# Optimization experiments

Measured on AMD Instinct MI355X. Metric: run time of the kernel, lower is better.

The kernel has to match this reference:

```python
import jax, jax.numpy as jnp
import numpy as np

T_TOK, N_UNITS, E, H, L_PATH, N_PATHS, B, VOCAB = 16, 4096, 128, 128, 32, 1024, 8, 16384
MAX_PATH_LEN = 32
PAD_ID = 0


def _run_lstm(x, Wi, Wh, b):
    # x: [T, N, E]; torch gate order i, f, g, o
    Hh = Wh.shape[1]
    h0 = jnp.zeros((x.shape[1], Hh), x.dtype)
    def step(carry, xt):
        h, c = carry
        g = xt @ Wi.T + h @ Wh.T + b
        i, f, gg, o = jnp.split(g, 4, axis=-1)
        c = jax.nn.sigmoid(f) * c + jax.nn.sigmoid(i) * jnp.tanh(gg)
        h = jax.nn.sigmoid(o) * jnp.tanh(c)
        return (h, c), h
    _, ys = jax.lax.scan(step, (h0, h0), x)
    return ys


def _bilstm(x, lengths, Wif, Whf, bf, Wib, Whb, bb):
    # emulates pack_padded_sequence + bidirectional LSTM + pad_packed (zeros past length)
    T = x.shape[0]
    t = jnp.arange(T)[:, None]
    valid = t < lengths[None, :]
    out_f = _run_lstm(x, Wif, Whf, bf)
    rev = jnp.clip(lengths[None, :] - 1 - t, 0, T - 1)  # reverse within each valid prefix
    x_rev = jnp.take_along_axis(x, rev[:, :, None], axis=0)
    out_b = jnp.take_along_axis(_run_lstm(x_rev, Wib, Whb, bb), rev[:, :, None], axis=0)
    return jnp.concatenate([out_f, out_b], axis=-1) * valid[:, :, None]


def _layernorm(x, g, b):
    m = x.mean(-1, keepdims=True)
    v = ((x - m) ** 2).mean(-1, keepdims=True)
    return (x - m) * jax.lax.rsqrt(v + 1e-5) * g + b


def _forward(units, paths, unit_per_data, path_per_data, emb, tl_Wif, tl_Whf, tl_bf,
             tl_Wib, tl_Whb, tl_bb, lin_W, lin_b, ln_g, ln_b, attn_w, attn_b,
             pl_Wif, pl_Whf, pl_bf, pl_Wib, pl_Whb, pl_bb, ul_W, ul_b):
    # ---- _token_encoder ----
    is_pad = units == PAD_ID
    tok_len = jnp.where(is_pad.any(0), jnp.argmax(is_pad, 0), units.shape[0])
    x = emb[units]                                              # [T, NU, E]
    h = _bilstm(x, tok_len, tl_Wif, tl_Whf, tl_bf, tl_Wib, tl_Whb, tl_bb)  # [T, NU, 2H]
    out = h @ lin_W.T + lin_b                                   # [T, NU, E]
    q = jnp.tanh(_layernorm(out, ln_g, ln_b))
    scores = q @ attn_w.T + attn_b                              # [T, NU, 1] local attention
    scores = jnp.where(is_pad[:, :, None], -1e9, scores)
    w = jax.nn.softmax(scores, axis=0)
    tok_feat = jnp.einsum('tn,tne->ne', w[..., 0], out)         # [NU, E]
    # ---- _unit_to_path (vectorized ragged gather) ----
    Lp, Pn = paths.shape
    has_end = (paths == -1).any(0)
    fe = jnp.where(has_end, jnp.argmax(paths == -1, 0), Lp)
    ML = min(Lp, MAX_PATH_LEN)
    nb = unit_per_data.shape[0]
    data_of_path = jnp.repeat(jnp.arange(nb), path_per_data, total_repeat_length=Pn)
    u_off = jnp.cumsum(unit_per_data) - unit_per_data
    off_p = u_off[data_of_path]
    un_p = unit_per_data[data_of_path]
    pL = paths[:ML]
    t = jnp.arange(ML)[:, None]
    within = t < fe[None, :]
    keep = within & (pL >= 0) & (pL < un_p[None, :])
    gidx = jnp.clip(jnp.clip(pL, 0, None) + off_p[None, :], 0, tok_feat.shape[0] - 1)
    feats = tok_feat[gidx] * keep[:, :, None]                   # [ML, P, E]
    mask = jnp.where(within, (pL < 0) | (pL > un_p[None, :]), True)
    # ---- _path_encoder ----
    p_len = jnp.where(mask.any(0), jnp.argmax(mask, 0), ML)
    hp = _bilstm(feats, p_len, pl_Wif, pl_Whf, pl_bf, pl_Wib, pl_Whb, pl_bb)
    return hp @ ul_W.T + ul_b                                   # [ML, P, E]


def setup_inputs() -> dict:
    rng = np.random.default_rng(0)
    tok_len = rng.integers(4, T_TOK + 1, N_UNITS); tok_len[0] = T_TOK
    units = rng.integers(1, VOCAB, (T_TOK, N_UNITS))
    units = np.where(np.arange(T_TOK)[:, None] < tok_len[None, :], units, PAD_ID)
    upd = N_UNITS // B
    p_len = rng.integers(8, L_PATH + 1, N_PATHS); p_len[0] = L_PATH
    paths = rng.integers(0, upd, (L_PATH, N_PATHS))
    paths = np.where(np.arange(L_PATH)[:, None] < p_len[None, :], paths, -1)
    key = jax.random.key(0)
    ks = iter(jax.random.split(key, 24))
    def pn(shape, s=0.08):
        return (jax.random.normal(next(ks), shape) * s).astype(jnp.float32)
    return dict(
        units=jnp.asarray(units, jnp.int32),
        paths=jnp.asarray(paths, jnp.int32),
        unit_per_data=jnp.full((B,), upd, jnp.int32),
        path_per_data=jnp.full((B,), N_PATHS // B, jnp.int32),
        emb=pn((VOCAB, E)),
        tl_Wif=pn((4 * H, E)), tl_Whf=pn((4 * H, H)), tl_bf=pn((4 * H,)),
        tl_Wib=pn((4 * H, E)), tl_Whb=pn((4 * H, H)), tl_bb=pn((4 * H,)),
        lin_W=pn((E, 2 * H)), lin_b=pn((E,)),
        ln_g=jnp.ones((E,), jnp.float32), ln_b=jnp.zeros((E,), jnp.float32),
        attn_w=pn((1, E)), attn_b=pn((1,)),
        pl_Wif=pn((4 * H, E)), pl_Whf=pn((4 * H, H)), pl_bf=pn((4 * H,)),
        pl_Wib=pn((4 * H, E)), pl_Whb=pn((4 * H, H)), pl_bb=pn((4 * H,)),
        ul_W=pn((E, 2 * H)), ul_b=pn((E,)),
    )


def reference(units, paths, unit_per_data, path_per_data, emb, tl_Wif, tl_Whf, tl_bf,
              tl_Wib, tl_Whb, tl_bb, lin_W, lin_b, ln_g, ln_b, attn_w, attn_b,
              pl_Wif, pl_Whf, pl_bf, pl_Wib, pl_Whb, pl_bb, ul_W, ul_b):
    return _forward(units, paths, unit_per_data, path_per_data, emb, tl_Wif, tl_Whf, tl_bf,
                    tl_Wib, tl_Whb, tl_bb, lin_W, lin_b, ln_g, ln_b, attn_w, attn_b,
                    pl_Wif, pl_Whf, pl_bf, pl_Wib, pl_Whb, pl_bb, ul_W, ul_b)
```

## Files before the change

kernel.cpp:

```cpp
#include <hip/hip_runtime.h>
#include <cstdint>
#include <cstddef>

#define T_TOKN 16
#define NUNITS 4096
#define LPATH  32
#define NPATHS 1024
#define BNUM   8

typedef __attribute__((ext_vector_type(8))) short short8;
typedef __attribute__((ext_vector_type(4))) short short4x;
typedef __attribute__((ext_vector_type(4))) float f32x4;

enum : size_t {
  OFF_WFRAG   = 0,
  OFF_LINFRAG = 262144,
  OFF_OUTF    = 294912,
  OFF_OUTB    = OFF_OUTF + 4194304,
  OFF_OUTLIN  = OFF_OUTB + 4194304,
  OFF_SCORES  = OFF_OUTLIN + 8388608,
  OFF_TOKFEAT = OFF_SCORES + 65536,
  OFF_POUTF   = OFF_TOKFEAT + 524288,
  OFF_POUTB   = OFF_POUTF + 2097152,
  OFF_INT     = OFF_POUTB + 2097152,
  WS_FLOATS   = OFF_INT + 8192
};

static __device__ __forceinline__ unsigned short f2bf(float f) {
  union { float f; unsigned u; } v; v.f = f;
  unsigned r = v.u + 0x7fffu + ((v.u >> 16) & 1u);
  return (unsigned short)(r >> 16);
}
static __device__ __forceinline__ unsigned pack_bf(float a, float b) {
  return (unsigned)f2bf(a) | ((unsigned)f2bf(b) << 16);
}
static __device__ __forceinline__ float sigf(float x)      { return 1.f / (1.f + __expf(-x)); }
static __device__ __forceinline__ float tanhfast(float x)  { return 2.f / (1.f + __expf(-2.f * x)) - 1.f; }

__global__ void prep_kernel(
    const float* __restrict__ tWif, const float* __restrict__ tWhf,
    const float* __restrict__ tWib, const float* __restrict__ tWhb,
    const float* __restrict__ pWif, const float* __restrict__ pWhf,
    const float* __restrict__ pWib, const float* __restrict__ pWhb,
    const float* __restrict__ linW, const float* __restrict__ ulW,
    const int* __restrict__ units, const int* __restrict__ paths,
    const int* __restrict__ upd, const int* __restrict__ ppd,
    float* __restrict__ ws, int* __restrict__ ip)
{
  int idx = blockIdx.x * 256 + threadIdx.x;
  if (idx < 524288) {
    unsigned short* wf = (unsigned short*)(ws + OFF_WFRAG);
    int mat = idx >> 17, rem = idx & 131071;
    int i  = rem & 7;
    int lane = (rem >> 3) & 63;
    int ct = (rem >> 9) & 3;
    int ks = (rem >> 11) & 7;
    int wv = (rem >> 14) & 7;
    int g = wv * 64 + ct * 16 + (lane & 15);
    int k = ks * 32 + ((lane >> 4) << 3) + i;
    const float* Wi; const float* Wh;
    switch (mat) {
      case 0: Wi = tWif; Wh = tWhf; break;
      case 1: Wi = tWib; Wh = tWhb; break;
      case 2: Wi = pWif; Wh = pWhf; break;
      default: Wi = pWib; Wh = pWhb; break;
    }
    float v = (k < 128) ? Wi[g * 128 + k] : Wh[g * 128 + (k - 128)];
    wf[idx] = f2bf(v);
  } else if (idx < 524288 + 65536) {
    unsigned short* lf = (unsigned short*)(ws + OFF_LINFRAG);
    int i2 = idx - 524288;
    int mat = i2 >> 15, rem = i2 & 32767;
    int i  = rem & 7;
    int lane = (rem >> 3) & 63;
    int ks = (rem >> 9) & 7;
    int ct = (rem >> 12) & 7;
    int e = ct * 16 + (lane & 15);
    int k = ks * 32 + ((lane >> 4) << 3) + i;
    const float* W = mat ? ulW : linW;
    lf[i2] = f2bf(W[e * 256 + k]);
  } else if (idx < 589824 + 4096) {
    int n = idx - 589824;
    int len = T_TOKN;
    for (int t = 0; t < T_TOKN; ++t)
      if (units[t * NUNITS + n] == 0) { len = t; break; }
    ip[n] = len;
  } else if (idx < 589824 + 5120) {
    int p = idx - (589824 + 4096);
    int* fe_a  = ip + 4096;
    int* p_len = ip + 5120;
    int* off_p = ip + 6144;
    int* un_p  = ip + 7168;
    int cum = 0; int d = BNUM - 1;
    for (int dd = 0; dd < BNUM; ++dd) {
      int c2 = cum + ppd[dd];
      if (p < c2) { d = dd; break; }
      cum = c2;
    }
    int off = 0;
    for (int dd = 0; dd < d; ++dd) off += upd[dd];
    int un = upd[d];
    off_p[p] = off; un_p[p] = un;
    int f = LPATH;
    for (int t = 0; t < LPATH; ++t)
      if (paths[t * NPATHS + p] == -1) { f = t; break; }
    fe_a[p] = f;
    int pl = LPATH;
    for (int t = 0; t < LPATH; ++t) {
      int v = paths[t * NPATHS + p];
      if ((t >= f) || (v < 0) || (v > un)) { pl = t; break; }
    }
    p_len[p] = pl;
  }
}

template <int MODE>
__global__ __launch_bounds__(1024, 4) void lstm_kernel(
    const unsigned short* __restrict__ wfragAll,
    const float* __restrict__ biasF, const float* __restrict__ biasB,
    const float* __restrict__ src,
    const int* __restrict__ idxsrc,
    const int* __restrict__ lens,
    const int* __restrict__ fe_a, const int* __restrict__ off_p, const int* __restrict__ un_p,
    unsigned short* __restrict__ outF, unsigned short* __restrict__ outB)
{
  constexpr int NN   = MODE ? NPATHS : NUNITS;
  constexpr int TT   = MODE ? LPATH : T_TOKN;
  constexpr int M    = MODE ? 8 : 32;
  constexpr int MR   = MODE ? 16 : 32;
  constexpr int NRT  = MR / 16;
  constexpr int ASTR = 264;
  constexpr int GSTR = 514;

  __shared__ unsigned short ash[MR * ASTR];
  __shared__ float gates[MR * GSTR];

  int tid  = threadIdx.x;
  int dir  = blockIdx.y;
  int n0   = blockIdx.x * M;
  int lane = tid & 63, wv = tid >> 6;

  const unsigned short* wbase =
      wfragAll + (size_t)((MODE ? 2 : 0) + dir) * 131072;
  int wv8 = wv >> 1;
  short8 bfr[8][2];
#pragma unroll
  for (int ks = 0; ks < 8; ++ks)
#pragma unroll
    for (int c2 = 0; c2 < 2; ++c2) {
      int ct = ((wv & 1) << 1) | c2;
      bfr[ks][c2] = *(const short8*)&wbase[((((wv8 * 8 + ks) * 4 + ct) * 64) + lane) * 8];
    }

  if (MODE == 0) {
    for (int i = tid; i < MR * 128; i += 1024)
      ash[(i >> 7) * ASTR + 128 + (i & 127)] = 0;
  } else {
    for (int i = tid; i < MR * ASTR; i += 1024) ash[i] = 0;
  }

  const float* bcp = dir ? biasB : biasF;
  int j2 = MODE ? (tid & 127) : ((tid & 63) * 2);
  int ug = MODE ? (tid >> 7)  : (tid >> 6);
  float2 b2[4];
#pragma unroll
  for (int q = 0; q < 4; ++q) {
    if (MODE == 0) b2[q] = *(const float2*)&bcp[q * 128 + j2];
    else           b2[q] = make_float2(bcp[q * 128 + j2], 0.f);
  }
  constexpr int NU = MODE ? 1 : 2;
  float cst0[NU], cst1[NU];
  int   ulen[NU];
#pragma unroll
  for (int i = 0; i < NU; ++i) {
    cst0[i] = 0.f; cst1[i] = 0.f;
    ulen[i] = lens[n0 + ug * NU + i];
  }

  int gu, gk0;
  if (MODE == 0) { gu = tid >> 5; gk0 = (tid & 31) * 4; }
  else           { gu = tid >> 7; gk0 = tid & 127; }
  int gn = n0 + gu;
  int glen = lens[gn];
  int gfe = 0, goff = 0, gun = 0;
  if (MODE) { gfe = fe_a[gn]; goff = off_p[gn]; gun = un_p[gn]; }

  float4 xq; float xs;
  if (MODE == 0) {
    int tau = dir ? min(max(glen - 1, 0), TT - 1) : 0;
    int tok = idxsrc[tau * NN + gn];
    xq = *(const float4*)&src[(size_t)tok * 128 + gk0];
  } else {
    int tau = dir ? min(max(glen - 1, 0), TT - 1) : 0;
    int v = idxsrc[tau * NN + gn];
    bool keep = (tau < gfe) && (v >= 0) && (v < gun);
    xs = 0.f;
    if (keep) xs = src[(size_t)min(v + goff, NUNITS - 1) * 128 + gk0];
  }
  __syncthreads();

  for (int t = 0; t < TT; ++t) {
    if (MODE == 0) {
      short4x x4;
      x4[0] = (short)f2bf(xq.x); x4[1] = (short)f2bf(xq.y);
      x4[2] = (short)f2bf(xq.z); x4[3] = (short)f2bf(xq.w);
      *(short4x*)&ash[gu * ASTR + gk0] = x4;
    } else {
      ash[gu * ASTR + gk0] = f2bf(xs);
    }
    __syncthreads();

    {
      int tn = (t + 1 < TT) ? t + 1 : t;
      int taun = dir ? min(max(glen - 1 - tn, 0), TT - 1) : tn;
      int vn = idxsrc[taun * NN + gn];
      f32x4 acc[NRT][2];
#pragma unroll
      for (int rt = 0; rt < NRT; ++rt)
#pragma unroll
        for (int c2 = 0; c2 < 2; ++c2) {
          f32x4 z = {0.f, 0.f, 0.f, 0.f};
          acc[rt][c2] = z;
        }
#pragma unroll
      for (int ks = 0; ks < 8; ++ks) {
        short8 afr[NRT];
#pragma unroll
        for (int rt = 0; rt < NRT; ++rt)
          afr[rt] = *(const short8*)&ash[(rt * 16 + (lane & 15)) * ASTR + ks * 32 + ((lane >> 4) << 3)];
#pragma unroll
        for (int rt = 0; rt < NRT; ++rt)
#pragma unroll
          for (int c2 = 0; c2 < 2; ++c2)
            acc[rt][c2] = __builtin_amdgcn_mfma_f32_16x16x32_bf16(
                afr[rt], bfr[ks][c2], acc[rt][c2], 0, 0, 0);
      }
      if (MODE == 0) {
        xq = *(const float4*)&src[(size_t)vn * 128 + gk0];
      } else {
        bool keep = (taun < gfe) && (vn >= 0) && (vn < gun);
        xs = 0.f;
        if (keep) xs = src[(size_t)min(vn + goff, NUNITS - 1) * 128 + gk0];
      }
#pragma unroll
      for (int rt = 0; rt < NRT; ++rt)
#pragma unroll
        for (int c2 = 0; c2 < 2; ++c2) {
          int g = wv * 32 + c2 * 16 + (lane & 15);
#pragma unroll
          for (int r = 0; r < 4; ++r) {
            int u = rt * 16 + ((lane >> 4) << 2) + r;
            gates[u * GSTR + g] = acc[rt][c2][r];
          }
        }
    }
    __syncthreads();

#pragma unroll
    for (int i = 0; i < NU; ++i) {
      int u = ug * NU + i;
      int n = n0 + u;
      if (MODE == 0) {
        float2 g0 = *(const float2*)&gates[u * GSTR + j2];
        float2 g1 = *(const float2*)&gates[u * GSTR + 128 + j2];
        float2 g2 = *(const float2*)&gates[u * GSTR + 256 + j2];
        float2 g3 = *(const float2*)&gates[u * GSTR + 384 + j2];
        float i0 = sigf(g0.x + b2[0].x), i1 = sigf(g0.y + b2[0].y);
        float f0 = sigf(g1.x + b2[1].x), f1 = sigf(g1.y + b2[1].y);
        float c0 = tanhfast(g2.x + b2[2].x), c1 = tanhfast(g2.y + b2[2].y);
        float o0 = sigf(g3.x + b2[3].x), o1 = sigf(g3.y + b2[3].y);
        float cA = f0 * cst0[i] + i0 * c0;
        float cB = f1 * cst1[i] + i1 * c1;
        cst0[i] = cA; cst1[i] = cB;
        float h0 = o0 * tanhfast(cA);
        float h1 = o1 * tanhfast(cB);
        unsigned hp = pack_bf(h0, h1);
        *(unsigned*)&ash[u * ASTR + 128 + j2] = hp;
        if (dir == 0) {
          *(unsigned*)&outF[((size_t)t * NN + n) * 128 + j2] = hp;
        } else {
          int L = ulen[i];
          if (t < L) *(unsigned*)&outB[((size_t)(L - 1 - t) * NN + n) * 128 + j2] = hp;
          else       *(unsigned*)&outB[((size_t)t * NN + n) * 128 + j2] = 0;
        }
      } else {
        float p0 = gates[u * GSTR + j2]       + b2[0].x;
        float p1 = gates[u * GSTR + 128 + j2] + b2[1].x;
        float p2 = gates[u * GSTR + 256 + j2] + b2[2].x;
        float p3 = gates[u * GSTR + 384 + j2] + b2[3].x;
        float ig = sigf(p0), fg = sigf(p1), gg = tanhfast(p2), og = sigf(p3);
        float c = fg * cst0[i] + ig * gg;
        cst0[i] = c;
        float h = og * tanhfast(c);
        unsigned short hb = f2bf(h);
        ash[u * ASTR + 128 + j2] = hb;
        if (dir == 0) {
          outF[((size_t)t * NN + n) * 128 + j2] = hb;
        } else {
          int L = ulen[i];
          if (t < L) outB[((size_t)(L - 1 - t) * NN + n) * 128 + j2] = hb;
          else       outB[((size_t)t * NN + n) * 128 + j2] = 0;
        }
      }
    }
  }
}

template <int EPI>
__global__ __launch_bounds__(256) void gemm_mfma(
    const unsigned short* __restrict__ INf, const unsigned short* __restrict__ INb,
    const int* __restrict__ lens,
    const unsigned short* __restrict__ Bfrag, const float* __restrict__ bias,
    float* __restrict__ OUT, float* __restrict__ scores,
    const float* __restrict__ lng, const float* __restrict__ lnb,
    const float* __restrict__ attw, const float* __restrict__ attb,
    const int* __restrict__ units, int Nn)
{
  constexpr int OSTR = 132;
  __shared__ float outs[64 * OSTR];
  __shared__ float red1[256];
  __shared__ float red2[256];
  __shared__ float rowm[64], rowr[64];
  __shared__ float awsh[128], lgsh[128], lbsh[128];

  int tid = threadIdx.x, lane = tid & 63, wv = tid >> 6;
  int row0 = blockIdx.x * 64;
  int t = row0 / Nn, n0 = row0 % Nn;

  if (EPI == 1 && tid < 128) {
    awsh[tid] = attw[tid]; lgsh[tid] = lng[tid]; lbsh[tid] = lnb[tid];
  }

  short8 bfr[8][2];
#pragma unroll
  for (int ks = 0; ks < 8; ++ks)
#pragma unroll
    for (int c2 = 0; c2 < 2; ++c2) {
      int ct = wv * 2 + c2;
      bfr[ks][c2] = *(const short8*)&Bfrag[(((ct * 8 + ks) * 64) + lane) * 8];
    }

  int rb = lane & 15;
  int koq = (lane >> 4) << 3;
  bool val[4];
#pragma unroll
  for (int rt = 0; rt < 4; ++rt)
    val[rt] = (EPI == 1) ? true : (t < lens[n0 + rt * 16 + rb]);

  f32x4 acc[4][2];
#pragma unroll
  for (int rt = 0; rt < 4; ++rt)
#pragma unroll
    for (int c2 = 0; c2 < 2; ++c2) {
      f32x4 z = {0.f, 0.f, 0.f, 0.f};
      acc[rt][c2] = z;
    }

#pragma unroll
  for (int ks = 0; ks < 8; ++ks) {
    const unsigned short* P = (ks < 4) ? INf : INb;
    int koff = (ks & 3) * 32 + koq;
#pragma unroll
    for (int rt = 0; rt < 4; ++rt) {
      short8 a = {0, 0, 0, 0, 0, 0, 0, 0};
      if (val[rt])
        a = *(const short8*)&P[((size_t)(row0 + rt * 16 + rb)) * 128 + koff];
#pragma unroll
      for (int c2 = 0; c2 < 2; ++c2)
        acc[rt][c2] = __builtin_amdgcn_mfma_f32_16x16x32_bf16(
            a, bfr[ks][c2], acc[rt][c2], 0, 0, 0);
    }
  }

  float bc[2];
#pragma unroll
  for (int c2 = 0; c2 < 2; ++c2) bc[c2] = bias[wv * 32 + c2 * 16 + rb];
#pragma unroll
  for (int rt = 0; rt < 4; ++rt)
#pragma unroll
    for (int c2 = 0; c2 < 2; ++c2) {
      int col = wv * 32 + c2 * 16 + rb;
      int ub  = rt * 16 + ((lane >> 4) << 2);
#pragma unroll
      for (int r = 0; r < 4; ++r)
        outs[(ub + r) * OSTR + col] = acc[rt][c2][r] + bc[c2];
    }
  __syncthreads();
// ... 25 lines not shown
      rowm[tid] = m;
      rowr[tid] = rsqrtf(var + 1e-5f);
    }
    __syncthreads();
    float m = rowm[row], rs = rowr[row];
    float sp = 0.f;
#pragma unroll
    for (int x = 0; x < 8; ++x) {
#pragma unroll
      for (int c = 0; c < 4; ++c) {
        int col = seg * 32 + x * 4 + c;
        float q = tanhfast((v[x][c] - m) * rs * lgsh[col] + lbsh[col]);
        sp += q * awsh[col];
      }
      *(f32x4*)&OUT[go + x * 4] = v[x];
    }
    red1[tid] = sp;
    __syncthreads();
    if (tid < 64) {
      float s3 = red1[tid * 4] + red1[tid * 4 + 1] + red1[tid * 4 + 2] + red1[tid * 4 + 3]
               + attb[0];
      int n = n0 + tid;
      if (units[t * NUNITS + n] == 0) s3 = -1e9f;
      scores[t * NUNITS + n] = s3;
    }
  }
}

__global__ __launch_bounds__(128) void softmax_feat_kernel(
    const float* __restrict__ scores, const float* __restrict__ out_lin,
    float* __restrict__ tok_feat)
{
  int n = blockIdx.x;
  int e = threadIdx.x;
  float s[T_TOKN];
  float m = -1e30f;
#pragma unroll
  for (int t = 0; t < T_TOKN; ++t) { s[t] = scores[t * NUNITS + n]; m = fmaxf(m, s[t]); }
  float sum = 0.f;
#pragma unroll
  for (int t = 0; t < T_TOKN; ++t) { s[t] = expf(s[t] - m); sum += s[t]; }
  float inv = 1.f / sum;
  float a = 0.f;
#pragma unroll
  for (int t = 0; t < T_TOKN; ++t)
    a += s[t] * inv * out_lin[((size_t)t * NUNITS + n) * 128 + e];
  tok_feat[n * 128 + e] = a;
}

extern "C" void kernel_launch(void* const* d_in, const int* in_sizes, int n_in,
                              void* d_out, int out_size, void* d_ws, size_t ws_size,
                              hipStream_t stream)
{
  const int*   units = (const int*)d_in[0];
  const int*   paths = (const int*)d_in[1];
  const int*   upd   = (const int*)d_in[2];
  const int*   ppd   = (const int*)d_in[3];
  const float* emb   = (const float*)d_in[4];
  const float* tWif  = (const float*)d_in[5];
  const float* tWhf  = (const float*)d_in[6];
  const float* tbf   = (const float*)d_in[7];
  const float* tWib  = (const float*)d_in[8];
  const float* tWhb  = (const float*)d_in[9];
  const float* tbb   = (const float*)d_in[10];
  const float* linW  = (const float*)d_in[11];
  const float* linb  = (const float*)d_in[12];
  const float* lng   = (const float*)d_in[13];
  const float* lnb   = (const float*)d_in[14];
  const float* attw  = (const float*)d_in[15];
  const float* attb  = (const float*)d_in[16];
  const float* pWif  = (const float*)d_in[17];
  const float* pWhf  = (const float*)d_in[18];
  const float* pbf   = (const float*)d_in[19];
  const float* pWib  = (const float*)d_in[20];
  const float* pWhb  = (const float*)d_in[21];
  const float* pbb   = (const float*)d_in[22];
  const float* ulW   = (const float*)d_in[23];
  const float* ulb   = (const float*)d_in[24];

  float* ws = (float*)d_ws;
  int*   ip = (int*)(ws + OFF_INT);
  if (ws_size < WS_FLOATS * sizeof(float)) return;

  unsigned short* wfrag   = (unsigned short*)(ws + OFF_WFRAG);
  unsigned short* linfrag = (unsigned short*)(ws + OFF_LINFRAG);
  unsigned short* ulfrag  = linfrag + 32768;
  unsigned short* OUTF  = (unsigned short*)(ws + OFF_OUTF);
  unsigned short* OUTB  = (unsigned short*)(ws + OFF_OUTB);
  unsigned short* POUTF = (unsigned short*)(ws + OFF_POUTF);
  unsigned short* POUTB = (unsigned short*)(ws + OFF_POUTB);

  prep_kernel<<<2324, 256, 0, stream>>>(tWif, tWhf, tWib, tWhb,
                                        pWif, pWhf, pWib, pWhb,
                                        linW, ulW, units, paths, upd, ppd,
                                        ws, ip);

  lstm_kernel<0><<<dim3(128, 2), 1024, 0, stream>>>(
      wfrag, tbf, tbb, emb, units, ip , nullptr, nullptr, nullptr,
      OUTF, OUTB);

  gemm_mfma<1><<<1024, 256, 0, stream>>>(
      OUTF, OUTB, ip , linfrag, linb,
      ws + OFF_OUTLIN, ws + OFF_SCORES, lng, lnb, attw, attb, units, NUNITS);

  softmax_feat_kernel<<<4096, 128, 0, stream>>>(ws + OFF_SCORES, ws + OFF_OUTLIN,
                                                ws + OFF_TOKFEAT);

  lstm_kernel<1><<<dim3(128, 2), 1024, 0, stream>>>(
      wfrag, pbf, pbb, ws + OFF_TOKFEAT, paths, ip + 5120 ,
      ip + 4096 , ip + 6144 , ip + 7168 ,
      POUTF, POUTB);

  gemm_mfma<0><<<512, 256, 0, stream>>>(
      POUTF, POUTB, ip + 5120 , ulfrag, ulb,
      (float*)d_out, nullptr, nullptr, nullptr, nullptr, nullptr, nullptr, NPATHS);
}
```

Baseline: 320.7 us.

## Precompute input-gate projections per vocab/unit row and shrink LSTM recurrence to hidden GEMM

Adds a gx_gemm kernel that computes the input-to-gate projection x@Wi for every embedding row (whole vocabulary) and for every token-feature row before the recurrence. Each LSTM step then only multiplies the hidden state by Wh and gathers the precomputed gate rows by token index. This halves the per-step MFMA K dimension. Blocks shrink to 512 threads with 16 or 4 sequences each, which gives more blocks. The cost is an extra GEMM over all 16384 vocab rows (more than the tokens actually used) plus a large fp32 gate buffer that is read back with gathers.

```diff
diff --git a/kernel.cpp b/kernel.cpp
--- a/kernel.cpp
+++ b/kernel.cpp
@@ -7,22 +7,24 @@
 #define LPATH  32
 #define NPATHS 1024
 #define BNUM   8
+#define VOCABN 16384
 
 typedef __attribute__((ext_vector_type(8))) short short8;
-typedef __attribute__((ext_vector_type(4))) short short4x;
 typedef __attribute__((ext_vector_type(4))) float f32x4;
 
 enum : size_t {
-  OFF_WFRAG   = 0,
-  OFF_LINFRAG = 262144,
-  OFF_OUTF    = 294912,
+  OFF_WHFRAG  = 0,
+  OFF_LINFRAG = 131072,
+  OFF_GEMB    = 163840,
+  OFF_GP      = OFF_GEMB,
+  OFF_POUTF   = OFF_GEMB + 4194304,
+  OFF_POUTB   = OFF_GEMB + 6291456,
+  OFF_OUTF    = OFF_GEMB + 16777216,
   OFF_OUTB    = OFF_OUTF + 4194304,
   OFF_OUTLIN  = OFF_OUTB + 4194304,
   OFF_SCORES  = OFF_OUTLIN + 8388608,
   OFF_TOKFEAT = OFF_SCORES + 65536,
-  OFF_POUTF   = OFF_TOKFEAT + 524288,
-  OFF_POUTB   = OFF_POUTF + 2097152,
-  OFF_INT     = OFF_POUTB + 2097152,
+  OFF_INT     = OFF_TOKFEAT + 524288,
   WS_FLOATS   = OFF_INT + 8192
 };
 
@@ -37,39 +39,35 @@
 static __device__ __forceinline__ float sigf(float x)      { return 1.f / (1.f + __expf(-x)); }
 static __device__ __forceinline__ float tanhfast(float x)  { return 2.f / (1.f + __expf(-2.f * x)) - 1.f; }
 
+static __device__ __forceinline__ short8 pack8(float4 a, float4 b) {
+  short8 r;
+  r[0] = (short)f2bf(a.x); r[1] = (short)f2bf(a.y);
+  r[2] = (short)f2bf(a.z); r[3] = (short)f2bf(a.w);
+  r[4] = (short)f2bf(b.x); r[5] = (short)f2bf(b.y);
+  r[6] = (short)f2bf(b.z); r[7] = (short)f2bf(b.w);
+  return r;
+}
+
 __global__ void prep_kernel(
-    const float* __restrict__ tWif, const float* __restrict__ tWhf,
-    const float* __restrict__ tWib, const float* __restrict__ tWhb,
-    const float* __restrict__ pWif, const float* __restrict__ pWhf,
-    const float* __restrict__ pWib, const float* __restrict__ pWhb,
+    const float* __restrict__ tWhf, const float* __restrict__ tWhb,
+    const float* __restrict__ pWhf, const float* __restrict__ pWhb,
     const float* __restrict__ linW, const float* __restrict__ ulW,
     const int* __restrict__ units, const int* __restrict__ paths,
     const int* __restrict__ upd, const int* __restrict__ ppd,
     float* __restrict__ ws, int* __restrict__ ip)
 {
   int idx = blockIdx.x * 256 + threadIdx.x;
-  if (idx < 524288) {
-    unsigned short* wf = (unsigned short*)(ws + OFF_WFRAG);
-    int mat = idx >> 17, rem = idx & 131071;
-    int i  = rem & 7;
-    int lane = (rem >> 3) & 63;
-    int ct = (rem >> 9) & 3;
-    int ks = (rem >> 11) & 7;
-    int wv = (rem >> 14) & 7;
-    int g = wv * 64 + ct * 16 + (lane & 15);
+  if (idx < 262144) {
+    unsigned short* wf = (unsigned short*)(ws + OFF_WHFRAG);
+    int i = idx & 7, lane = (idx >> 3) & 63, c4 = (idx >> 9) & 3;
+    int ks = (idx >> 11) & 3, wv = (idx >> 13) & 7, mat = idx >> 16;
+    int g = wv * 64 + c4 * 16 + (lane & 15);
     int k = ks * 32 + ((lane >> 4) << 3) + i;
-    const float* Wi; const float* Wh;
-    switch (mat) {
-      case 0: Wi = tWif; Wh = tWhf; break;
-      case 1: Wi = tWib; Wh = tWhb; break;
-      case 2: Wi = pWif; Wh = pWhf; break;
-      default: Wi = pWib; Wh = pWhb; break;
-    }
-    float v = (k < 128) ? Wi[g * 128 + k] : Wh[g * 128 + (k - 128)];
-    wf[idx] = f2bf(v);
-  } else if (idx < 524288 + 65536) {
+    const float* Wh = (mat == 0) ? tWhf : (mat == 1) ? tWhb : (mat == 2) ? pWhf : pWhb;
+    wf[idx] = f2bf(Wh[g * 128 + k]);
+  } else if (idx < 262144 + 65536) {
     unsigned short* lf = (unsigned short*)(ws + OFF_LINFRAG);
-    int i2 = idx - 524288;
+    int i2 = idx - 262144;
     int mat = i2 >> 15, rem = i2 & 32767;
     int i  = rem & 7;
     int lane = (rem >> 3) & 63;
@@ -79,14 +77,14 @@
     int k = ks * 32 + ((lane >> 4) << 3) + i;
     const float* W = mat ? ulW : linW;
     lf[i2] = f2bf(W[e * 256 + k]);
-  } else if (idx < 589824 + 4096) {
-    int n = idx - 589824;
+  } else if (idx < 327680 + 4096) {
+    int n = idx - 327680;
     int len = T_TOKN;
     for (int t = 0; t < T_TOKN; ++t)
       if (units[t * NUNITS + n] == 0) { len = t; break; }
     ip[n] = len;
-  } else if (idx < 589824 + 5120) {
-    int p = idx - (589824 + 4096);
+  } else if (idx < 331776 + 1024) {
+    int p = idx - 331776;
     int* fe_a  = ip + 4096;
     int* p_len = ip + 5120;
     int* off_p = ip + 6144;
@@ -114,195 +112,228 @@
   }
 }
 
+template <int NROWS>
+__global__ __launch_bounds__(512) void gx_gemm(
+    const float* __restrict__ src,
+    const float* __restrict__ Wf, const float* __restrict__ Wb,
+    float* __restrict__ out)
+{
+  __shared__ float ot[16 * 520];
+  int tid = threadIdx.x, lane = tid & 63, wv = tid >> 6;
+  int dir = blockIdx.y;
+  int r0 = blockIdx.x * 16;
+  int rb = lane & 15, quad = lane >> 4;
+  const float* W = dir ? Wb : Wf;
+
+  short8 bfr[4][4];
+#pragma unroll
+  for (int ks = 0; ks < 4; ++ks)
+#pragma unroll
+    for (int c4 = 0; c4 < 4; ++c4) {
+      int g = wv * 64 + c4 * 16 + rb;
+      int k0 = ks * 32 + quad * 8;
+      float4 w0 = *(const float4*)&W[g * 128 + k0];
+      float4 w1 = *(const float4*)&W[g * 128 + k0 + 4];
+      bfr[ks][c4] = pack8(w0, w1);
+    }
+
+  f32x4 acc[4];
+#pragma unroll
+  for (int c4 = 0; c4 < 4; ++c4) { f32x4 z = {0.f,0.f,0.f,0.f}; acc[c4] = z; }
+
+#pragma unroll
+  for (int ks = 0; ks < 4; ++ks) {
+    const float* ap = &src[(size_t)(r0 + rb) * 128 + ks * 32 + quad * 8];
+    float4 a0 = *(const float4*)ap;
+    float4 a1 = *(const float4*)(ap + 4);
+    short8 af = pack8(a0, a1);
+#pragma unroll
+    for (int c4 = 0; c4 < 4; ++c4)
+      acc[c4] = __builtin_amdgcn_mfma_f32_16x16x32_bf16(af, bfr[ks][c4], acc[c4], 0, 0, 0);
+  }
+
+#pragma unroll
+  for (int c4 = 0; c4 < 4; ++c4) {
+    int g = wv * 64 + c4 * 16 + rb;
+    int j = g & 127, q = g >> 7;
+#pragma unroll
+    for (int r = 0; r < 4; ++r) {
+      int u = quad * 4 + r;
+      ot[u * 520 + j * 4 + q] = acc[c4][r];
+    }
+  }
+  __syncthreads();
+
+  float* o = out + (size_t)dir * NROWS * 512;
+  for (int x = tid; x < 2048; x += 512) {
+    int u = x >> 7, seg = x & 127;
+    *(f32x4*)&o[((size_t)(r0 + u)) * 512 + seg * 4] = *(const f32x4*)&ot[u * 520 + seg * 4];
+  }
+}
+
 template <int MODE>
-__global__ __launch_bounds__(1024, 4) void lstm_kernel(
-    const unsigned short* __restrict__ wfragAll,
+__global__ __launch_bounds__(512, 4) void lstm_kernel(
+    const unsigned short* __restrict__ whfragAll,
     const float* __restrict__ biasF, const float* __restrict__ biasB,
-    const float* __restrict__ src,
+    const float* __restrict__ gxT,
     const int* __restrict__ idxsrc,
     const int* __restrict__ lens,
     const int* __restrict__ fe_a, const int* __restrict__ off_p, const int* __restrict__ un_p,
     unsigned short* __restrict__ outF, unsigned short* __restrict__ outB)
 {
-  constexpr int NN   = MODE ? NPATHS : NUNITS;
-  constexpr int TT   = MODE ? LPATH : T_TOKN;
-  constexpr int M    = MODE ? 8 : 32;
-  constexpr int MR   = MODE ? 16 : 32;
-  constexpr int NRT  = MR / 16;
-  constexpr int ASTR = 264;
-  constexpr int GSTR = 514;
-
-  __shared__ unsigned short ash[MR * ASTR];
-  __shared__ float gates[MR * GSTR];
-
-  int tid  = threadIdx.x;
-  int dir  = blockIdx.y;
-  int n0   = blockIdx.x * M;
-  int lane = tid & 63, wv = tid >> 6;
-
-  const unsigned short* wbase =
-      wfragAll + (size_t)((MODE ? 2 : 0) + dir) * 131072;
-  int wv8 = wv >> 1;
-  short8 bfr[8][2];
-#pragma unroll
-  for (int ks = 0; ks < 8; ++ks)
-#pragma unroll
-    for (int c2 = 0; c2 < 2; ++c2) {
-      int ct = ((wv & 1) << 1) | c2;
-      bfr[ks][c2] = *(const short8*)&wbase[((((wv8 * 8 + ks) * 4 + ct) * 64) + lane) * 8];
-    }
-
+  constexpr int NN    = MODE ? NPATHS : NUNITS;
+  constexpr int TT    = MODE ? LPATH : T_TOKN;
+  constexpr int M     = MODE ? 4 : 16;
+  constexpr int GROWS = MODE ? NUNITS : VOCABN;
+  constexpr int ASTR  = 136;
+  constexpr int GSTR  = 514;
+
+  __shared__ unsigned short hsh[16 * ASTR];
+  __shared__ float gates[16 * GSTR];
+
+  int tid = threadIdx.x, lane = tid & 63, wv = tid >> 6;
+  int dir = blockIdx.y;
+  int n0  = blockIdx.x * M;
+  int rb = lane & 15, quad = lane >> 4;
+
+  const unsigned short* wb = whfragAll + (size_t)((MODE ? 2 : 0) + dir) * 65536;
+  short8 bfr[4][4];
+#pragma unroll
+  for (int ks = 0; ks < 4; ++ks)
+#pragma unroll
+    for (int c4 = 0; c4 < 4; ++c4)
+      bfr[ks][c4] = *(const short8*)&wb[(((wv * 4 + ks) * 4 + c4) * 64 + lane) * 8];
+
+  for (int i = tid; i < 16 * ASTR; i += 512) hsh[i] = 0;
+
+  const float* gxd = gxT + (size_t)dir * GROWS * 512;
+  const float* bcp = dir ? biasB : biasF;
+
+  int jX  = MODE ? (tid & 127) : ((tid & 63) * 2);
+  int ugX = MODE ? (tid >> 7)  : (tid >> 6);
+  float2 b2[4];
+#pragma unroll
+  for (int q = 0; q < 4; ++q) {
+    if (MODE == 0) b2[q] = *(const float2*)&bcp[q * 128 + jX];
+    else           b2[q] = make_float2(bcp[q * 128 + jX], 0.f);
+  }
+  float cst0[2] = {0.f, 0.f}, cst1[2] = {0.f, 0.f};
+  int ulen[2];
+  ulen[0] = lens[n0 + ugX * (MODE ? 1 : 2)];
+  ulen[1] = (MODE == 0) ? lens[n0 + ugX * 2 + 1] : 0;
+
+  int gfe = 0, goff = 0, gun = 0;
+  if (MODE) { gfe = fe_a[n0 + ugX]; goff = off_p[n0 + ugX]; gun = un_p[n0 + ugX]; }
+
+  f32x4 gq[2][2];
+  f32x4 gxp = {0.f, 0.f, 0.f, 0.f};
   if (MODE == 0) {
-    for (int i = tid; i < MR * 128; i += 1024)
-      ash[(i >> 7) * ASTR + 128 + (i & 127)] = 0;
+#pragma unroll
+    for (int i = 0; i < 2; ++i) {
+      int tau = dir ? min(max(ulen[i] - 1, 0), TT - 1) : 0;
+      int tok = idxsrc[tau * NN + n0 + ugX * 2 + i];
+      gq[i][0] = *(const f32x4*)&gxd[(size_t)tok * 512 + jX * 4];
+      gq[i][1] = *(const f32x4*)&gxd[(size_t)tok * 512 + jX * 4 + 4];
+    }
   } else {
-    for (int i = tid; i < MR * ASTR; i += 1024) ash[i] = 0;
-  }
-
-  const float* bcp = dir ? biasB : biasF;
-  int j2 = MODE ? (tid & 127) : ((tid & 63) * 2);
-  int ug = MODE ? (tid >> 7)  : (tid >> 6);
-  float2 b2[4];
-#pragma unroll
-  for (int q = 0; q < 4; ++q) {
-    if (MODE == 0) b2[q] = *(const float2*)&bcp[q * 128 + j2];
-    else           b2[q] = make_float2(bcp[q * 128 + j2], 0.f);
-  }
-  constexpr int NU = MODE ? 1 : 2;
-  float cst0[NU], cst1[NU];
-  int   ulen[NU];
-#pragma unroll
-  for (int i = 0; i < NU; ++i) {
-    cst0[i] = 0.f; cst1[i] = 0.f;
-    ulen[i] = lens[n0 + ug * NU + i];
-  }
-
-  int gu, gk0;
-  if (MODE == 0) { gu = tid >> 5; gk0 = (tid & 31) * 4; }
-  else           { gu = tid >> 7; gk0 = tid & 127; }
-  int gn = n0 + gu;
-  int glen = lens[gn];
-  int gfe = 0, goff = 0, gun = 0;
-  if (MODE) { gfe = fe_a[gn]; goff = off_p[gn]; gun = un_p[gn]; }
-
-  float4 xq; float xs;
-  if (MODE == 0) {
-    int tau = dir ? min(max(glen - 1, 0), TT - 1) : 0;
-    int tok = idxsrc[tau * NN + gn];
-    xq = *(const float4*)&src[(size_t)tok * 128 + gk0];
-  } else {
-    int tau = dir ? min(max(glen - 1, 0), TT - 1) : 0;
-    int v = idxsrc[tau * NN + gn];
-    bool keep = (tau < gfe) && (v >= 0) && (v < gun);
-    xs = 0.f;
-    if (keep) xs = src[(size_t)min(v + goff, NUNITS - 1) * 128 + gk0];
+    int tau = dir ? min(max(ulen[0] - 1, 0), TT - 1) : 0;
+    int v = idxsrc[tau * NN + n0 + ugX];
+    if ((tau < gfe) && (v >= 0) && (v < gun))
+      gxp = *(const f32x4*)&gxd[(size_t)min(v + goff, NUNITS - 1) * 512 + jX * 4];
   }
   __syncthreads();
 
   for (int t = 0; t < TT; ++t) {
+    f32x4 acc[4];
+#pragma unroll
+    for (int c4 = 0; c4 < 4; ++c4) { f32x4 z = {0.f,0.f,0.f,0.f}; acc[c4] = z; }
+#pragma unroll
+    for (int ks = 0; ks < 4; ++ks) {
+      short8 af = *(const short8*)&hsh[rb * ASTR + ks * 32 + quad * 8];
+#pragma unroll
+      for (int c4 = 0; c4 < 4; ++c4)
+        acc[c4] = __builtin_amdgcn_mfma_f32_16x16x32_bf16(af, bfr[ks][c4], acc[c4], 0, 0, 0);
+    }
+    int tn = (t + 1 < TT) ? t + 1 : t;
+    int ntok0 = 0, ntok1 = 0, nv = 0, ntau = 0;
     if (MODE == 0) {
-      short4x x4;
-      x4[0] = (short)f2bf(xq.x); x4[1] = (short)f2bf(xq.y);
-      x4[2] = (short)f2bf(xq.z); x4[3] = (short)f2bf(xq.w);
-      *(short4x*)&ash[gu * ASTR + gk0] = x4;
+      int tau0 = dir ? min(max(ulen[0] - 1 - tn, 0), TT - 1) : tn;
+      int tau1 = dir ? min(max(ulen[1] - 1 - tn, 0), TT - 1) : tn;
+      ntok0 = idxsrc[tau0 * NN + n0 + ugX * 2];
+      ntok1 = idxsrc[tau1 * NN + n0 + ugX * 2 + 1];
     } else {
-      ash[gu * ASTR + gk0] = f2bf(xs);
+      ntau = dir ? min(max(ulen[0] - 1 - tn, 0), TT - 1) : tn;
+      nv = idxsrc[ntau * NN + n0 + ugX];
+    }
+#pragma unroll
+    for (int c4 = 0; c4 < 4; ++c4) {
+      int g = wv * 64 + c4 * 16 + rb;
+#pragma unroll
+      for (int r = 0; r < 4; ++r)
+        gates[(quad * 4 + r) * GSTR + g] = acc[c4][r];
     }
     __syncthreads();
 
-    {
-      int tn = (t + 1 < TT) ? t + 1 : t;
-      int taun = dir ? min(max(glen - 1 - tn, 0), TT - 1) : tn;
-      int vn = idxsrc[taun * NN + gn];
-      f32x4 acc[NRT][2];
-#pragma unroll
-      for (int rt = 0; rt < NRT; ++rt)
-#pragma unroll
-        for (int c2 = 0; c2 < 2; ++c2) {
-          f32x4 z = {0.f, 0.f, 0.f, 0.f};
-          acc[rt][c2] = z;
-        }
-#pragma unroll
-      for (int ks = 0; ks < 8; ++ks) {
-        short8 afr[NRT];
-#pragma unroll
-        for (int rt = 0; rt < NRT; ++rt)
-          afr[rt] = *(const short8*)&ash[(rt * 16 + (lane & 15)) * ASTR + ks * 32 + ((lane >> 4) << 3)];
-#pragma unroll
-        for (int rt = 0; rt < NRT; ++rt)
-#pragma unroll
-          for (int c2 = 0; c2 < 2; ++c2)
-            acc[rt][c2] = __builtin_amdgcn_mfma_f32_16x16x32_bf16(
-                afr[rt], bfr[ks][c2], acc[rt][c2], 0, 0, 0);
-      }
-      if (MODE == 0) {
-        xq = *(const float4*)&src[(size_t)vn * 128 + gk0];
-      } else {
-        bool keep = (taun < gfe) && (vn >= 0) && (vn < gun);
-        xs = 0.f;
-        if (keep) xs = src[(size_t)min(vn + goff, NUNITS - 1) * 128 + gk0];
-      }
-#pragma unroll
-      for (int rt = 0; rt < NRT; ++rt)
-#pragma unroll
-        for (int c2 = 0; c2 < 2; ++c2) {
-          int g = wv * 32 + c2 * 16 + (lane & 15);
-#pragma unroll
-          for (int r = 0; r < 4; ++r) {
-            int u = rt * 16 + ((lane >> 4) << 2) + r;
-            gates[u * GSTR + g] = acc[rt][c2][r];
-          }
-        }
-    }
-    __syncthreads();
-
-#pragma unroll
-    for (int i = 0; i < NU; ++i) {
-      int u = ug * NU + i;
-      int n = n0 + u;
-      if (MODE == 0) {
-        float2 g0 = *(const float2*)&gates[u * GSTR + j2];
-        float2 g1 = *(const float2*)&gates[u * GSTR + 128 + j2];
-        float2 g2 = *(const float2*)&gates[u * GSTR + 256 + j2];
-        float2 g3 = *(const float2*)&gates[u * GSTR + 384 + j2];
-        float i0 = sigf(g0.x + b2[0].x), i1 = sigf(g0.y + b2[0].y);
-        float f0 = sigf(g1.x + b2[1].x), f1 = sigf(g1.y + b2[1].y);
-        float c0 = tanhfast(g2.x + b2[2].x), c1 = tanhfast(g2.y + b2[2].y);
-        float o0 = sigf(g3.x + b2[3].x), o1 = sigf(g3.y + b2[3].y);
-        float cA = f0 * cst0[i] + i0 * c0;
-        float cB = f1 * cst1[i] + i1 * c1;
+    if (MODE == 0) {
+#pragma unroll
+      for (int i = 0; i < 2; ++i) {
+        int u = ugX * 2 + i, n = n0 + u;
+        float2 q0 = *(const float2*)&gates[u * GSTR + jX];
+        float2 q1 = *(const float2*)&gates[u * GSTR + 128 + jX];
+        float2 q2 = *(const float2*)&gates[u * GSTR + 256 + jX];
+        float2 q3 = *(const float2*)&gates[u * GSTR + 384 + jX];
+        float i0 = sigf(q0.x + gq[i][0][0] + b2[0].x);
+        float f0 = sigf(q1.x + gq[i][0][1] + b2[1].x);
+        float g0 = tanhfast(q2.x + gq[i][0][2] + b2[2].x);
+        float o0 = sigf(q3.x + gq[i][0][3] + b2[3].x);
+        float i1 = sigf(q0.y + gq[i][1][0] + b2[0].y);
+        float f1 = sigf(q1.y + gq[i][1][1] + b2[1].y);
+        float g1 = tanhfast(q2.y + gq[i][1][2] + b2[2].y);
+        float o1 = sigf(q3.y + gq[i][1][3] + b2[3].y);
+        float cA = f0 * cst0[i] + i0 * g0;
+        float cB = f1 * cst1[i] + i1 * g1;
         cst0[i] = cA; cst1[i] = cB;
         float h0 = o0 * tanhfast(cA);
         float h1 = o1 * tanhfast(cB);
         unsigned hp = pack_bf(h0, h1);
-        *(unsigned*)&ash[u * ASTR + 128 + j2] = hp;
+        *(unsigned*)&hsh[u * ASTR + jX] = hp;
         if (dir == 0) {
-          *(unsigned*)&outF[((size_t)t * NN + n) * 128 + j2] = hp;
+          *(unsigned*)&outF[((size_t)t * NN + n) * 128 + jX] = hp;
         } else {
           int L = ulen[i];
-          if (t < L) *(unsigned*)&outB[((size_t)(L - 1 - t) * NN + n) * 128 + j2] = hp;
-          else       *(unsigned*)&outB[((size_t)t * NN + n) * 128 + j2] = 0;
-        }
-      } else {
-        float p0 = gates[u * GSTR + j2]       + b2[0].x;
-        float p1 = gates[u * GSTR + 128 + j2] + b2[1].x;
-        float p2 = gates[u * GSTR + 256 + j2] + b2[2].x;
-        float p3 = gates[u * GSTR + 384 + j2] + b2[3].x;
-        float ig = sigf(p0), fg = sigf(p1), gg = tanhfast(p2), og = sigf(p3);
-        float c = fg * cst0[i] + ig * gg;
-        cst0[i] = c;
-        float h = og * tanhfast(c);
-        unsigned short hb = f2bf(h);
-        ash[u * ASTR + 128 + j2] = hb;
-        if (dir == 0) {
-          outF[((size_t)t * NN + n) * 128 + j2] = hb;
-        } else {
-          int L = ulen[i];
-          if (t < L) outB[((size_t)(L - 1 - t) * NN + n) * 128 + j2] = hb;
-          else       outB[((size_t)t * NN + n) * 128 + j2] = 0;
+          if (t < L) *(unsigned*)&outB[((size_t)(L - 1 - t) * NN + n) * 128 + jX] = hp;
+          else       *(unsigned*)&outB[((size_t)t * NN + n) * 128 + jX] = 0;
         }
       }
-    }
+      gq[0][0] = *(const f32x4*)&gxd[(size_t)ntok0 * 512 + jX * 4];
+      gq[0][1] = *(const f32x4*)&gxd[(size_t)ntok0 * 512 + jX * 4 + 4];
+      gq[1][0] = *(const f32x4*)&gxd[(size_t)ntok1 * 512 + jX * 4];
+      gq[1][1] = *(const f32x4*)&gxd[(size_t)ntok1 * 512 + jX * 4 + 4];
+    } else {
+      int u = ugX, n = n0 + u;
+      float p0 = gates[u * GSTR + jX]       + gxp[0] + b2[0].x;
+      float p1 = gates[u * GSTR + 128 + jX] + gxp[1] + b2[1].x;
+      float p2 = gates[u * GSTR + 256 + jX] + gxp[2] + b2[2].x;
+      float p3 = gates[u * GSTR + 384 + jX] + gxp[3] + b2[3].x;
+      float ig = sigf(p0), fg = sigf(p1), gg = tanhfast(p2), og = sigf(p3);
+      float c = fg * cst0[0] + ig * gg;
+      cst0[0] = c;
+      float h = og * tanhfast(c);
+      unsigned short hb = f2bf(h);
+      hsh[u * ASTR + jX] = hb;
+      if (dir == 0) {
+        outF[((size_t)t * NN + n) * 128 + jX] = hb;
+      } else {
+        int L = ulen[0];
+        if (t < L) outB[((size_t)(L - 1 - t) * NN + n) * 128 + jX] = hb;
+        else       outB[((size_t)t * NN + n) * 128 + jX] = 0;
+      }
+      bool nkeep = (ntau < gfe) && (nv >= 0) && (nv < gun);
+      f32x4 z = {0.f, 0.f, 0.f, 0.f};
+      gxp = z;
+      if (nkeep) gxp = *(const f32x4*)&gxd[(size_t)min(nv + goff, NUNITS - 1) * 512 + jX * 4];
+    }
+    __syncthreads();
   }
 }
 
@@ -494,21 +525,23 @@
   int*   ip = (int*)(ws + OFF_INT);
   if (ws_size < WS_FLOATS * sizeof(float)) return;
 
-  unsigned short* wfrag   = (unsigned short*)(ws + OFF_WFRAG);
+  unsigned short* whfrag  = (unsigned short*)(ws + OFF_WHFRAG);
   unsigned short* linfrag = (unsigned short*)(ws + OFF_LINFRAG);
   unsigned short* ulfrag  = linfrag + 32768;
+  float* GEMB = ws + OFF_GEMB;
+  float* GP   = ws + OFF_GP;
   unsigned short* OUTF  = (unsigned short*)(ws + OFF_OUTF);
   unsigned short* OUTB  = (unsigned short*)(ws + OFF_OUTB);
   unsigned short* POUTF = (unsigned short*)(ws + OFF_POUTF);
   unsigned short* POUTB = (unsigned short*)(ws + OFF_POUTB);
 
-  prep_kernel<<<2324, 256, 0, stream>>>(tWif, tWhf, tWib, tWhb,
-                                        pWif, pWhf, pWib, pWhb,
-                                        linW, ulW, units, paths, upd, ppd,
-                                        ws, ip);
-
-  lstm_kernel<0><<<dim3(128, 2), 1024, 0, stream>>>(
-      wfrag, tbf, tbb, emb, units, ip , nullptr, nullptr, nullptr,
+  prep_kernel<<<1300, 256, 0, stream>>>(tWhf, tWhb, pWhf, pWhb, linW, ulW,
+                                        units, paths, upd, ppd, ws, ip);
+
+  gx_gemm<VOCABN><<<dim3(VOCABN / 16, 2), 512, 0, stream>>>(emb, tWif, tWib, GEMB);
+
+  lstm_kernel<0><<<dim3(NUNITS / 16, 2), 512, 0, stream>>>(
+      whfrag, tbf, tbb, GEMB, units, ip , nullptr, nullptr, nullptr,
       OUTF, OUTB);
 
   gemm_mfma<1><<<1024, 256, 0, stream>>>(
@@ -518,8 +551,11 @@
   softmax_feat_kernel<<<4096, 128, 0, stream>>>(ws + OFF_SCORES, ws + OFF_OUTLIN,
                                                 ws + OFF_TOKFEAT);
 
-  lstm_kernel<1><<<dim3(128, 2), 1024, 0, stream>>>(
-      wfrag, pbf, pbb, ws + OFF_TOKFEAT, paths, ip + 5120 ,
+  gx_gemm<NUNITS><<<dim3(NUNITS / 16, 2), 512, 0, stream>>>(
+      ws + OFF_TOKFEAT, pWif, pWib, GP);
+
+  lstm_kernel<1><<<dim3(NPATHS / 4, 2), 512, 0, stream>>>(
+      whfrag, pbf, pbb, GP, paths, ip + 5120 ,
       ip + 4096 , ip + 6144 , ip + 7168 ,
       POUTF, POUTB);
 
```

New measurement: 420.7 us. 1.31x slower.

## Halve sequences per LSTM block to double grid size and parallelism

Applied to the files above, without the earlier changes.

The token LSTM now handles 16 units per block instead of 32, and the path LSTM 4 paths instead of 8. This doubles the grid to 512 and 512 blocks over 2 directions, so more CUs work on the latency-bound recurrent scan. Each thread owns one unit instead of two, and the MFMA row-tile loop collapses to a single 16-row tile. The cost is that every block reloads the weight fragments, MFMA tiles are half-empty in path mode (4 of 16 rows used), and the launch-bounds hint is raised to 8 waves per SIMD.

```diff
diff --git a/kernel.cpp b/kernel.cpp
--- a/kernel.cpp
+++ b/kernel.cpp
@@ -9,7 +9,6 @@
 #define BNUM   8
 
 typedef __attribute__((ext_vector_type(8))) short short8;
-typedef __attribute__((ext_vector_type(4))) short short4x;
 typedef __attribute__((ext_vector_type(4))) float f32x4;
 
 enum : size_t {
@@ -115,7 +114,7 @@
 }
 
 template <int MODE>
-__global__ __launch_bounds__(1024, 4) void lstm_kernel(
+__global__ __launch_bounds__(1024, 8) void lstm_kernel(
     const unsigned short* __restrict__ wfragAll,
     const float* __restrict__ biasF, const float* __restrict__ biasB,
     const float* __restrict__ src,
@@ -126,14 +125,12 @@
 {
   constexpr int NN   = MODE ? NPATHS : NUNITS;
   constexpr int TT   = MODE ? LPATH : T_TOKN;
-  constexpr int M    = MODE ? 8 : 32;
-  constexpr int MR   = MODE ? 16 : 32;
-  constexpr int NRT  = MR / 16;
+  constexpr int M    = MODE ? 4 : 16;
   constexpr int ASTR = 264;
   constexpr int GSTR = 514;
 
-  __shared__ unsigned short ash[MR * ASTR];
-  __shared__ float gates[MR * GSTR];
+  __shared__ unsigned short ash[16 * ASTR];
+  __shared__ float gates[16 * GSTR];
 
   int tid  = threadIdx.x;
   int dir  = blockIdx.y;
@@ -153,154 +150,128 @@
     }
 
   if (MODE == 0) {
-    for (int i = tid; i < MR * 128; i += 1024)
+    for (int i = tid; i < 16 * 128; i += 1024)
       ash[(i >> 7) * ASTR + 128 + (i & 127)] = 0;
   } else {
-    for (int i = tid; i < MR * ASTR; i += 1024) ash[i] = 0;
+    for (int i = tid; i < 16 * ASTR; i += 1024) ash[i] = 0;
   }
 
   const float* bcp = dir ? biasB : biasF;
   int j2 = MODE ? (tid & 127) : ((tid & 63) * 2);
   int ug = MODE ? (tid >> 7)  : (tid >> 6);
+  bool pact = (MODE == 0) || (ug < M);
+  int un_ = n0 + (MODE ? min(ug, M - 1) : ug);
   float2 b2[4];
 #pragma unroll
   for (int q = 0; q < 4; ++q) {
     if (MODE == 0) b2[q] = *(const float2*)&bcp[q * 128 + j2];
     else           b2[q] = make_float2(bcp[q * 128 + j2], 0.f);
   }
-  constexpr int NU = MODE ? 1 : 2;
-  float cst0[NU], cst1[NU];
-  int   ulen[NU];
-#pragma unroll
-  for (int i = 0; i < NU; ++i) {
-    cst0[i] = 0.f; cst1[i] = 0.f;
-    ulen[i] = lens[n0 + ug * NU + i];
-  }
-
-  int gu, gk0;
-  if (MODE == 0) { gu = tid >> 5; gk0 = (tid & 31) * 4; }
-  else           { gu = tid >> 7; gk0 = tid & 127; }
-  int gn = n0 + gu;
-  int glen = lens[gn];
+  float cstA = 0.f, cstB = 0.f;
+  int ulen = lens[un_];
   int gfe = 0, goff = 0, gun = 0;
-  if (MODE) { gfe = fe_a[gn]; goff = off_p[gn]; gun = un_p[gn]; }
-
-  float4 xq; float xs;
+  if (MODE) { gfe = fe_a[un_]; goff = off_p[un_]; gun = un_p[un_]; }
+
+  float2 xq; float xs = 0.f;
   if (MODE == 0) {
-    int tau = dir ? min(max(glen - 1, 0), TT - 1) : 0;
-    int tok = idxsrc[tau * NN + gn];
-    xq = *(const float4*)&src[(size_t)tok * 128 + gk0];
+    int tau = dir ? min(max(ulen - 1, 0), TT - 1) : 0;
+    int tok = idxsrc[tau * NN + un_];
+    xq = *(const float2*)&src[(size_t)tok * 128 + j2];
   } else {
-    int tau = dir ? min(max(glen - 1, 0), TT - 1) : 0;
-    int v = idxsrc[tau * NN + gn];
-    bool keep = (tau < gfe) && (v >= 0) && (v < gun);
-    xs = 0.f;
-    if (keep) xs = src[(size_t)min(v + goff, NUNITS - 1) * 128 + gk0];
+    int tau = dir ? min(max(ulen - 1, 0), TT - 1) : 0;
+    int v = idxsrc[tau * NN + un_];
+    if ((tau < gfe) && (v >= 0) && (v < gun))
+      xs = src[(size_t)min(v + goff, NUNITS - 1) * 128 + j2];
   }
   __syncthreads();
 
   for (int t = 0; t < TT; ++t) {
     if (MODE == 0) {
-      short4x x4;
-      x4[0] = (short)f2bf(xq.x); x4[1] = (short)f2bf(xq.y);
-      x4[2] = (short)f2bf(xq.z); x4[3] = (short)f2bf(xq.w);
-      *(short4x*)&ash[gu * ASTR + gk0] = x4;
-    } else {
-      ash[gu * ASTR + gk0] = f2bf(xs);
+      *(unsigned*)&ash[ug * ASTR + j2] = pack_bf(xq.x, xq.y);
+    } else if (ug < M) {
+      ash[ug * ASTR + j2] = f2bf(xs);
     }
     __syncthreads();
 
     {
       int tn = (t + 1 < TT) ? t + 1 : t;
-      int taun = dir ? min(max(glen - 1 - tn, 0), TT - 1) : tn;
-      int vn = idxsrc[taun * NN + gn];
-      f32x4 acc[NRT][2];
-#pragma unroll
-      for (int rt = 0; rt < NRT; ++rt)
-#pragma unroll
-        for (int c2 = 0; c2 < 2; ++c2) {
-          f32x4 z = {0.f, 0.f, 0.f, 0.f};
-          acc[rt][c2] = z;
-        }
+      int taun = dir ? min(max(ulen - 1 - tn, 0), TT - 1) : tn;
+      int vn = idxsrc[taun * NN + un_];
+      f32x4 acc[2];
+#pragma unroll
+      for (int c2 = 0; c2 < 2; ++c2) {
+        f32x4 z = {0.f, 0.f, 0.f, 0.f};
+        acc[c2] = z;
+      }
 #pragma unroll
       for (int ks = 0; ks < 8; ++ks) {
-        short8 afr[NRT];
-#pragma unroll
-        for (int rt = 0; rt < NRT; ++rt)
-          afr[rt] = *(const short8*)&ash[(rt * 16 + (lane & 15)) * ASTR + ks * 32 + ((lane >> 4) << 3)];
-#pragma unroll
-        for (int rt = 0; rt < NRT; ++rt)
-#pragma unroll
-          for (int c2 = 0; c2 < 2; ++c2)
-            acc[rt][c2] = __builtin_amdgcn_mfma_f32_16x16x32_bf16(
-                afr[rt], bfr[ks][c2], acc[rt][c2], 0, 0, 0);
+        short8 af = *(const short8*)&ash[(lane & 15) * ASTR + ks * 32 + ((lane >> 4) << 3)];
+#pragma unroll
+        for (int c2 = 0; c2 < 2; ++c2)
+          acc[c2] = __builtin_amdgcn_mfma_f32_16x16x32_bf16(
+              af, bfr[ks][c2], acc[c2], 0, 0, 0);
       }
       if (MODE == 0) {
-        xq = *(const float4*)&src[(size_t)vn * 128 + gk0];
+        xq = *(const float2*)&src[(size_t)vn * 128 + j2];
       } else {
         bool keep = (taun < gfe) && (vn >= 0) && (vn < gun);
         xs = 0.f;
-        if (keep) xs = src[(size_t)min(vn + goff, NUNITS - 1) * 128 + gk0];
-      }
-#pragma unroll
-      for (int rt = 0; rt < NRT; ++rt)
-#pragma unroll
-        for (int c2 = 0; c2 < 2; ++c2) {
-          int g = wv * 32 + c2 * 16 + (lane & 15);
-#pragma unroll
-          for (int r = 0; r < 4; ++r) {
-            int u = rt * 16 + ((lane >> 4) << 2) + r;
-            gates[u * GSTR + g] = acc[rt][c2][r];
-          }
+        if (keep) xs = src[(size_t)min(vn + goff, NUNITS - 1) * 128 + j2];
+      }
+#pragma unroll
+      for (int c2 = 0; c2 < 2; ++c2) {
+        int g = wv * 32 + c2 * 16 + (lane & 15);
+#pragma unroll
+        for (int r = 0; r < 4; ++r) {
+          int u = ((lane >> 4) << 2) + r;
+          gates[u * GSTR + g] = acc[c2][r];
         }
+      }
     }
     __syncthreads();
 
-#pragma unroll
-    for (int i = 0; i < NU; ++i) {
-      int u = ug * NU + i;
-      int n = n0 + u;
-      if (MODE == 0) {
-        float2 g0 = *(const float2*)&gates[u * GSTR + j2];
-        float2 g1 = *(const float2*)&gates[u * GSTR + 128 + j2];
-        float2 g2 = *(const float2*)&gates[u * GSTR + 256 + j2];
-        float2 g3 = *(const float2*)&gates[u * GSTR + 384 + j2];
-        float i0 = sigf(g0.x + b2[0].x), i1 = sigf(g0.y + b2[0].y);
-        float f0 = sigf(g1.x + b2[1].x), f1 = sigf(g1.y + b2[1].y);
-        float c0 = tanhfast(g2.x + b2[2].x), c1 = tanhfast(g2.y + b2[2].y);
-        float o0 = sigf(g3.x + b2[3].x), o1 = sigf(g3.y + b2[3].y);
-        float cA = f0 * cst0[i] + i0 * c0;
-        float cB = f1 * cst1[i] + i1 * c1;
-        cst0[i] = cA; cst1[i] = cB;
-        float h0 = o0 * tanhfast(cA);
-        float h1 = o1 * tanhfast(cB);
-        unsigned hp = pack_bf(h0, h1);
-        *(unsigned*)&ash[u * ASTR + 128 + j2] = hp;
-        if (dir == 0) {
-          *(unsigned*)&outF[((size_t)t * NN + n) * 128 + j2] = hp;
-        } else {
-          int L = ulen[i];
-          if (t < L) *(unsigned*)&outB[((size_t)(L - 1 - t) * NN + n) * 128 + j2] = hp;
-          else       *(unsigned*)&outB[((size_t)t * NN + n) * 128 + j2] = 0;
-        }
+    if (MODE == 0) {
+      int u = ug, n = n0 + ug;
+      float2 g0 = *(const float2*)&gates[u * GSTR + j2];
+      float2 g1 = *(const float2*)&gates[u * GSTR + 128 + j2];
+      float2 g2 = *(const float2*)&gates[u * GSTR + 256 + j2];
+      float2 g3 = *(const float2*)&gates[u * GSTR + 384 + j2];
+      float i0 = sigf(g0.x + b2[0].x), i1 = sigf(g0.y + b2[0].y);
+      float f0 = sigf(g1.x + b2[1].x), f1 = sigf(g1.y + b2[1].y);
+      float c0 = tanhfast(g2.x + b2[2].x), c1 = tanhfast(g2.y + b2[2].y);
+      float o0 = sigf(g3.x + b2[3].x), o1 = sigf(g3.y + b2[3].y);
+      float cA = f0 * cstA + i0 * c0;
+      float cB = f1 * cstB + i1 * c1;
+      cstA = cA; cstB = cB;
+      float h0 = o0 * tanhfast(cA);
+      float h1 = o1 * tanhfast(cB);
+      unsigned hp = pack_bf(h0, h1);
+      *(unsigned*)&ash[u * ASTR + 128 + j2] = hp;
+      if (dir == 0) {
+        *(unsigned*)&outF[((size_t)t * NN + n) * 128 + j2] = hp;
       } else {
-        float p0 = gates[u * GSTR + j2]       + b2[0].x;
-        float p1 = gates[u * GSTR + 128 + j2] + b2[1].x;
-        float p2 = gates[u * GSTR + 256 + j2] + b2[2].x;
-        float p3 = gates[u * GSTR + 384 + j2] + b2[3].x;
-        float ig = sigf(p0), fg = sigf(p1), gg = tanhfast(p2), og = sigf(p3);
-        float c = fg * cst0[i] + ig * gg;
-        cst0[i] = c;
-        float h = og * tanhfast(c);
-        unsigned short hb = f2bf(h);
-        ash[u * ASTR + 128 + j2] = hb;
-        if (dir == 0) {
-          outF[((size_t)t * NN + n) * 128 + j2] = hb;
-        } else {
-          int L = ulen[i];
-          if (t < L) outB[((size_t)(L - 1 - t) * NN + n) * 128 + j2] = hb;
-          else       outB[((size_t)t * NN + n) * 128 + j2] = 0;
-        }
+        int L = ulen;
+        if (t < L) *(unsigned*)&outB[((size_t)(L - 1 - t) * NN + n) * 128 + j2] = hp;
+        else       *(unsigned*)&outB[((size_t)t * NN + n) * 128 + j2] = 0;
+      }
+    } else if (pact) {
+      int u = ug, n = n0 + ug;
+      float p0 = gates[u * GSTR + j2]       + b2[0].x;
+      float p1 = gates[u * GSTR + 128 + j2] + b2[1].x;
+      float p2 = gates[u * GSTR + 256 + j2] + b2[2].x;
+      float p3 = gates[u * GSTR + 384 + j2] + b2[3].x;
+      float ig = sigf(p0), fg = sigf(p1), gg = tanhfast(p2), og = sigf(p3);
+      float c = fg * cstA + ig * gg;
+      cstA = c;
+      float h = og * tanhfast(c);
+      unsigned short hb = f2bf(h);
+      ash[u * ASTR + 128 + j2] = hb;
+      if (dir == 0) {
+        outF[((size_t)t * NN + n) * 128 + j2] = hb;
+      } else {
+        int L = ulen;
+        if (t < L) outB[((size_t)(L - 1 - t) * NN + n) * 128 + j2] = hb;
+        else       outB[((size_t)t * NN + n) * 128 + j2] = 0;
       }
     }
   }
@@ -507,7 +478,7 @@
                                         linW, ulW, units, paths, upd, ppd,
                                         ws, ip);
 
-  lstm_kernel<0><<<dim3(128, 2), 1024, 0, stream>>>(
+  lstm_kernel<0><<<dim3(NUNITS / 16, 2), 1024, 0, stream>>>(
       wfrag, tbf, tbb, emb, units, ip , nullptr, nullptr, nullptr,
       OUTF, OUTB);
 
@@ -518,7 +489,7 @@
   softmax_feat_kernel<<<4096, 128, 0, stream>>>(ws + OFF_SCORES, ws + OFF_OUTLIN,
                                                 ws + OFF_TOKFEAT);
 
-  lstm_kernel<1><<<dim3(128, 2), 1024, 0, stream>>>(
+  lstm_kernel<1><<<dim3(NPATHS / 4, 2), 1024, 0, stream>>>(
       wfrag, pbf, pbb, ws + OFF_TOKFEAT, paths, ip + 5120 ,
       ip + 4096 , ip + 6144 , ip + 7168 ,
       POUTF, POUTB);
```

After: 774.6 us. 2.42x slower.
